# Kernel optimization log

Measured on AMD Instinct MI355X. Metric: run time of the kernel, lower is better.

## Reference

```python
import jax, jax.numpy as jnp
import numpy as np
import math

MU = 5; ETA = 1.0; ITERS = 3
SIGMA_C = 1.0; SIGMA_S = 1.6 * SIGMA_C
SIGMA_M = 3.0; RHO = 0.99; TAU = 0.7
MAX_T = int(math.floor(3 * SIGMA_C))  # 3
MAX_S = int(math.floor(3 * SIGMA_M))  # 9
DELTA = 1.0
B, C, X, Y = 4, 1, 512, 512


def _gpdf(v, sig):
    return math.exp(-v * v / (2.0 * sig * sig)) / (math.sqrt(2.0 * math.pi) * sig)


def _sobel(img):
    k = jnp.array([[-1., -2., -1.], [0., 0., 0.], [1., 2., 1.]], dtype=img.dtype)
    kern = jnp.stack([k, k.T])[:, None]  # [2,1,3,3] OIHW
    return jax.lax.conv_general_dilated(img, kern, (1, 1), [(1, 1), (1, 1)],
                                        dimension_numbers=('NCHW', 'OIHW', 'NCHW'))


def _gather_flat(arr, idx):
    # arr [b,c,x,y], idx int [b,x,y] flattened spatial index (px*Y+py)
    b, c, x, y = arr.shape
    flat = arr.reshape(b, c, x * y)
    idxb = jnp.broadcast_to(idx.reshape(b, 1, x * y), (b, c, x * y))
    return jnp.take_along_axis(flat, idxb, axis=2).reshape(b, c, x, y)


def _safe_norm(v):
    m = jnp.linalg.norm(v, axis=1, keepdims=True)
    return v / jnp.where(m == 0, 1.0, m)


def _etf(images):
    b, c, x, y = images.shape
    sob = _sobel(images)                                   # [b,2,x,y]
    mag = jnp.linalg.norm(sob, axis=1, keepdims=True)      # [b,1,x,y]
    mag = mag / jnp.max(mag)
    mag_p = jnp.pad(mag, ((0, 0), (0, 0), (MU, MU), (MU, MU)))
    sobel_X = mag[:, None]                                 # [b,1,1,x,y]
    tang = _safe_norm(jnp.stack([-sob[:, 1], sob[:, 0]], axis=1))
    K = 2 * MU + 1
    for _ in range(ITERS):
        for ori in ('V', 'H'):
            tang_p = jnp.pad(tang, ((0, 0), (0, 0), (MU, MU), (MU, MU)))
            tang_X = tang[:, None]                         # [b,1,2,x,y]
            if ori == 'V':
                tang_Y = jnp.stack([tang_p[:, :, i:i + x, MU:MU + y] for i in range(K)], axis=1)
                sobel_Y = jnp.stack([mag_p[:, :, i:i + x, MU:MU + y] for i in range(K)], axis=1)
            else:
                tang_Y = jnp.stack([tang_p[:, :, MU:MU + x, i:i + y] for i in range(K)], axis=1)
                sobel_Y = jnp.stack([mag_p[:, :, MU:MU + x, i:i + y] for i in range(K)], axis=1)
            # weight: magnitude term * direction term / 2
            w = (jnp.tanh(ETA * (sobel_Y - sobel_X)) + 1.0) \
                * jnp.sum(tang_X * tang_Y, axis=2, keepdims=True) * 0.5
            tang = _safe_norm(jnp.sum(tang_Y * w, axis=1))
    return tang


def _dog(images, etf):
    b, c, x, y = images.shape
    xi, yi = jnp.meshgrid(jnp.arange(x, dtype=images.dtype),
                          jnp.arange(y, dtype=images.dtype), indexing='ij')
    idx0 = jnp.broadcast_to(jnp.stack([xi, yi])[None], (b, 2, x, y))
    per = jnp.stack([-etf[:, 1], etf[:, 0]], axis=1)       # perpendicular to flow
    dog = jnp.zeros_like(images)
    tw = 0.0
    for t in range(-MAX_T, MAX_T + 1):
        pts = idx0 + DELTA * per * t
        px = jnp.round(jnp.clip(pts[:, 0], 0, x - 1)).astype(jnp.int32)
        py = jnp.round(jnp.clip(pts[:, 1], 0, y - 1)).astype(jnp.int32)
        il = _gather_flat(images, px * y + py)
        gw = _gpdf(t, SIGMA_C) - RHO * _gpdf(t, SIGMA_S)
        tw += gw
        dog = dog + il * gw
    return dog / tw


def _fdog_float(images):
    b, c, x, y = images.shape
    etf = _etf(images)
    dog = _dog(images, etf)
    fdog = jnp.zeros_like(images)
    tw = 0.0
    xi, yi = jnp.meshgrid(jnp.arange(x, dtype=jnp.int32),
                          jnp.arange(y, dtype=jnp.int32), indexing='ij')
    for s_dir in (-1, 1):
        px = jnp.broadcast_to(xi[None], (b, x, y))
        py = jnp.broadcast_to(yi[None], (b, x, y))
        for s in range(0 if s_dir == 1 else 1, MAX_S + 1):
            if s != 0:
                p_etf = _gather_flat(etf, px * y + py)     # flow at current points
                fx = px.astype(images.dtype) + DELTA * p_etf[:, 0] * s_dir
                fy = py.astype(images.dtype) + DELTA * p_etf[:, 1] * s_dir
                px = jnp.round(jnp.clip(fx, 0, x - 1)).astype(jnp.int32)
                py = jnp.round(jnp.clip(fy, 0, y - 1)).astype(jnp.int32)
            f_s = _gather_flat(dog, px * y + py)
            gw = _gpdf(s, SIGMA_M)
            tw += gw
            fdog = fdog + f_s * gw
    return fdog / tw


def setup_inputs() -> dict:
    key = jax.random.key(0)
    images = jax.random.uniform(key, (B, C, X, Y), dtype=jnp.float32)
    return {"images": images}


def reference(images):
    fdog = _fdog_float(images)
    edges = ~((fdog < 0) & (1.0 + jnp.tanh(fdog) < TAU))
    return edges.astype(jnp.int32)
```

## Files before the change

### kernel.cpp

```cpp
#include <hip/hip_runtime.h>
#include <math.h>

#pragma clang fp contract(off)

#define BN 4
#define SX 512
#define SY 512
#define NPIX (BN * SX * SY)
#define MU 5
#define MB (1024 * 1024)
#define SOB_BLOCKS (NPIX / 1024)

struct DogW  { float g[7];  float tw; };
struct FdogW { float g[10]; float tw; };

__device__ __forceinline__ float fast_tanh_f32(float dF) {
    double d = (double)dF;
    double y = fabs(d);
    double t = expm1(2.0 * y);
    double r = t / (t + 2.0);
    if (y > 350.0) r = 1.0;
    return (float)copysign(r, d);
}

__device__ __forceinline__ float img_at(const float* __restrict__ img, int b, int x, int y) {
    if (x < 0 || x >= SX || y < 0 || y >= SY) return 0.0f;
    return img[(size_t)b * SX * SY + (size_t)x * SY + y];
}

__global__ __launch_bounds__(256) void k_sobel(const float* __restrict__ img,
                                               float* __restrict__ mag,
                                               float2* __restrict__ tang,
                                               float* __restrict__ partial) {
#pragma clang fp contract(off)
    int tid = threadIdx.x;
    size_t pixbase = (size_t)blockIdx.x * 1024 + (size_t)tid * 4;
    int b  = (int)(pixbase >> 18);
    int p  = (int)(pixbase & 262143);
    int xi = p >> 9;
    int yi = p & 511;
    size_t base = (size_t)b * SX * SY;
    size_t idx  = base + (size_t)xi * SY + yi;

    bool xm = (xi - 1 >= 0);
    bool xp = (xi + 1 < SX);
    const float* rowm = img + base + (size_t)(xi - 1) * SY;
    const float* row0 = img + base + (size_t)xi * SY;
    const float* rowp = img + base + (size_t)(xi + 1) * SY;

    float4 a4 = make_float4(0.f, 0.f, 0.f, 0.f);
    float4 c4 = make_float4(0.f, 0.f, 0.f, 0.f);
    float4 b4 = *(const float4*)(row0 + yi);
    if (xm) a4 = *(const float4*)(rowm + yi);
    if (xp) c4 = *(const float4*)(rowp + yi);

    float aL = 0.f, aR = 0.f, bL = 0.f, bR = 0.f, cL = 0.f, cR = 0.f;
    if (yi > 0) {
        bL = row0[yi - 1];
        if (xm) aL = rowm[yi - 1];
        if (xp) cL = rowp[yi - 1];
    }
    if (yi + 4 < SY) {
        bR = row0[yi + 4];
        if (xm) aR = rowm[yi + 4];
        if (xp) cR = rowp[yi + 4];
    }

    float a[6] = { aL, a4.x, a4.y, a4.z, a4.w, aR };
    float bb[6] = { bL, b4.x, b4.y, b4.z, b4.w, bR };
    float c[6] = { cL, c4.x, c4.y, c4.z, c4.w, cR };

    float4 m4;
    float4 t01, t23;
    float wm = 0.0f;
#pragma unroll
    for (int j = 0; j < 4; ++j) {
        float v00 = a[j];
        float v01 = a[j + 1];
        float v02 = a[j + 2];
        float v10 = bb[j];
        float v12 = bb[j + 2];
        float v20 = c[j];
        float v21 = c[j + 1];
        float v22 = c[j + 2];

        float s0 = (-1.0f * v00);
        s0 = s0 + (-2.0f * v01);
        s0 = s0 + (-1.0f * v02);
        s0 = s0 + ( 1.0f * v20);
        s0 = s0 + ( 2.0f * v21);
        s0 = s0 + ( 1.0f * v22);
        float s1 = (-1.0f * v00);
        s1 = s1 + ( 1.0f * v02);
        s1 = s1 + (-2.0f * v10);
        s1 = s1 + ( 2.0f * v12);
        s1 = s1 + (-1.0f * v20);
        s1 = s1 + ( 1.0f * v22);

        float m = sqrtf((s0 * s0) + (s1 * s1));
        float tx = -s1, ty = s0;
        float n = sqrtf((tx * tx) + (ty * ty));
        float d = (n == 0.0f) ? 1.0f : n;
        float ex = tx / d;
        float ey = ty / d;

        (&m4.x)[j] = m;
        if (j == 0) { t01.x = ex; t01.y = ey; }
        if (j == 1) { t01.z = ex; t01.w = ey; }
        if (j == 2) { t23.x = ex; t23.y = ey; }
        if (j == 3) { t23.z = ex; t23.w = ey; }
        wm = fmaxf(wm, m);
    }
    *(float4*)(mag + idx) = m4;
    ((float4*)(tang + idx))[0] = t01;
    ((float4*)(tang + idx))[1] = t23;

    for (int off = 32; off > 0; off >>= 1) wm = fmaxf(wm, __shfl_down(wm, off, 64));
    __shared__ float red[4];
    int lane = tid & 63;
    int wid  = tid >> 6;
    if (lane == 0) red[wid] = wm;
    __syncthreads();
    if (tid == 0)
        partial[blockIdx.x] = fmaxf(fmaxf(red[0], red[1]), fmaxf(red[2], red[3]));
}

__global__ void k_reduce(const float* __restrict__ partial, unsigned int* __restrict__ maxbits) {
    float m = 0.0f;
    for (int i = threadIdx.x; i < SOB_BLOCKS; i += 256) m = fmaxf(m, partial[i]);
    for (int off = 32; off > 0; off >>= 1) m = fmaxf(m, __shfl_down(m, off, 64));
    __shared__ float red[4];
    int lane = threadIdx.x & 63;
    int wid  = threadIdx.x >> 6;
    if (lane == 0) red[wid] = m;
    __syncthreads();
    if (threadIdx.x == 0) {
        float bm = fmaxf(fmaxf(red[0], red[1]), fmaxf(red[2], red[3]));
        *maxbits = __float_as_uint(bm);
    }
}

__global__ void k_norm(float* __restrict__ mag, const unsigned int* __restrict__ maxbits) {
    int i = blockIdx.x * blockDim.x + threadIdx.x;
    float mx = __uint_as_float(*maxbits);
    mag[i] = mag[i] / mx;
}

__global__ void k_tanh(const float* __restrict__ mag, const float* __restrict__ partial,
                       float* __restrict__ TV, float* __restrict__ TH) {
#pragma clang fp contract(off)
    int tid = threadIdx.x;
    float m2 = 0.0f;
    for (int i = tid; i < SOB_BLOCKS; i += 256) m2 = fmaxf(m2, partial[i]);
    for (int off = 32; off > 0; off >>= 1) m2 = fmaxf(m2, __shfl_down(m2, off, 64));
    __shared__ float red[4];
    int lane = tid & 63;
    int wid  = tid >> 6;
    if (lane == 0) red[wid] = m2;
    __syncthreads();
    const float mx = fmaxf(fmaxf(red[0], red[1]), fmaxf(red[2], red[3]));

    int yi = blockIdx.x * blockDim.x + tid;
    int xi = blockIdx.y;
    int b  = blockIdx.z;
    size_t base = (size_t)b * SX * SY;
    size_t idx  = base + (size_t)xi * SY + yi;
    float cm = mag[idx] / mx;
#pragma unroll
    for (int k = 1; k <= 5; ++k) {
        if (xi + k < SX) {
            float nm = mag[idx + (size_t)k * SY] / mx;
            TV[(size_t)(k - 1) * NPIX + idx] = fast_tanh_f32(nm - cm);
        }
    }
#pragma unroll
    for (int k = 1; k <= 5; ++k) {
        if (yi + k < SY) {
            float nm = mag[idx + k] / mx;
            TH[(size_t)(k - 1) * NPIX + idx] = fast_tanh_f32(nm - cm);
        }
    }
}

#define VTY 32
#define VTX 16
__global__ __launch_bounds__(256) void k_etf_v(const float2* __restrict__ tsrc,
                                               float2* __restrict__ tdst,
                                               const float* __restrict__ TV) {
#pragma clang fp contract(off)
    int ty  = threadIdx.x & 31;
    int txw = threadIdx.x >> 5;
    int y0 = blockIdx.x * VTY;
    int x0 = blockIdx.y * VTX;
    int b  = blockIdx.z;
    size_t base = (size_t)b * SX * SY;

    __shared__ __align__(16) float2 sT[VTX + 2 * MU][VTY];
    __shared__ __align__(16) float  sTV[5][VTX + MU][VTY];

    int tid = threadIdx.x;
    for (int i = tid; i < (VTX + 2 * MU) * (VTY / 4) * 2; i += 256) {
        int r = i >> 4;
        int c = i & 15;
        int gx = x0 - MU + r;
        if (gx >= 0 && gx < SX)
            ((float4*)&sT[r][0])[c] = ((const float4*)(tsrc + base + (size_t)gx * SY + y0))[c];
    }
    for (int i = tid; i < 5 * (VTX + MU) * (VTY / 4); i += 256) {
        int j   = i / ((VTX + MU) * (VTY / 4));
        int rem = i - j * ((VTX + MU) * (VTY / 4));
        int r   = rem >> 3;
        int c   = rem & 7;
        int gx  = x0 - MU + r;
        if (gx >= 0 && gx < SX)
            ((float4*)&sTV[j][r][0])[c] =
                ((const float4*)(TV + (size_t)j * NPIX + base + (size_t)gx * SY + y0))[c];
    }
    __syncthreads();

    int yi = y0 + ty;
#pragma unroll
    for (int sub = 0; sub < 2; ++sub) {
        int tx = txw + (sub << 3);
        int xi = x0 + tx;
        size_t idx = base + (size_t)xi * SY + yi;

        float2 ct = sT[tx + MU][ty];
        float sx = 0.0f, sy = 0.0f;
#pragma unroll
        for (int k = -MU; k <= MU; ++k) {
            int nx = xi + k;
            if (nx < 0 || nx >= SX) continue;
            float2 nt = sT[tx + MU + k][ty];
            float th;
            if (k > 0)      th =  sTV[k - 1][tx + MU][ty];
            else if (k < 0) th = -sTV[-k - 1][tx + MU + k][ty];
            else            th =  0.0f;
            float dot = (ct.x * nt.x) + (ct.y * nt.y);
            float w   = ((th + 1.0f) * dot) * 0.5f;
            sx = sx + (nt.x * w);
            sy = sy + (nt.y * w);
        }
        float n = sqrtf((sx * sx) + (sy * sy));
        float d = (n == 0.0f) ? 1.0f : n;
        tdst[idx] = make_float2(sx / d, sy / d);
    }
}

__global__ __launch_bounds__(256) void k_etf_h(const float2* __restrict__ tsrc,
                                               float2* __restrict__ tdst,
                                               const float* __restrict__ TH,
                                               const float* __restrict__ img,
                                               float* __restrict__ dogout,
                                               DogW dw, int do_dog) {
#pragma clang fp contract(off)
    int tid = threadIdx.x;
    int xi  = blockIdx.y;
    int b   = blockIdx.z;
    size_t base    = (size_t)b * SX * SY;
    size_t rowbase = base + (size_t)xi * SY;

    __shared__ __align__(16) float2 sT[SY];
    __shared__ __align__(16) float  sTH[5][SY];

    ((float4*)sT)[tid] = ((const float4*)(tsrc + rowbase))[tid];
    for (int i = tid; i < 5 * (SY / 4); i += 256) {
        int j = i >> 7;
        int c = i & 127;
        ((float4*)&sTH[0][0])[i] = ((const float4*)(TH + (size_t)j * NPIX + rowbase))[c];
    }
    __syncthreads();

#pragma unroll
    for (int half = 0; half < 2; ++half) {
        int yi = tid + half * 256;
        float2 ct = sT[yi];
        float sx = 0.0f, sy = 0.0f;
#pragma unroll
        for (int k = -MU; k <= MU; ++k) {
            int ny = yi + k;
            if (ny < 0 || ny >= SY) continue;
            float2 nt = sT[ny];
            float th;
            if (k > 0)      th =  sTH[k - 1][yi];
            else if (k < 0) th = -sTH[-k - 1][ny];
            else            th =  0.0f;
            float dot = (ct.x * nt.x) + (ct.y * nt.y);
            float w   = ((th + 1.0f) * dot) * 0.5f;
            sx = sx + (nt.x * w);
            sy = sy + (nt.y * w);
        }
        float n = sqrtf((sx * sx) + (sy * sy));
        float d = (n == 0.0f) ? 1.0f : n;
        float ex = sx / d;
        float ey = sy / d;
        tdst[rowbase + yi] = make_float2(ex, ey);

        if (do_dog) {
            float perx = -ey;
            float pery =  ex;
            float xf = (float)xi, yf = (float)yi;
            float acc = 0.0f;
#pragma unroll
            for (int t = -3; t <= 3; ++t) {
                float tf  = (float)t;
                float ptx = xf + (perx * tf);
                float pty = yf + (pery * tf);
                int px = (int)rintf(fminf(fmaxf(ptx, 0.0f), (float)(SX - 1)));
                int py = (int)rintf(fminf(fmaxf(pty, 0.0f), (float)(SY - 1)));
                float il = img[base + (size_t)px * SY + py];
                acc = acc + (il * dw.g[t + 3]);
            }
            dogout[rowbase + yi] = acc / dw.tw;
        }
    }
}

__global__ void k_etf(const float2* __restrict__ tsrc, float2* __restrict__ tdst,
                      const float* __restrict__ mag, int vert) {
#pragma clang fp contract(off)
    int yi = blockIdx.x * blockDim.x + threadIdx.x;
    int xi = blockIdx.y;
    int b  = blockIdx.z;
    size_t base = (size_t)b * SX * SY;
    size_t idx  = base + (size_t)xi * SY + yi;

    float  cm = mag[idx];
    float2 ct = tsrc[idx];

    float sx = 0.0f, sy = 0.0f;
    for (int k = -MU; k <= MU; ++k) {
        int nx = xi + (vert ? k : 0);
        int ny = yi + (vert ? 0 : k);
        if (nx < 0 || nx >= SX || ny < 0 || ny >= SY) continue;
        size_t nidx = base + (size_t)nx * SY + ny;
        float  nm = mag[nidx];
        float2 nt = tsrc[nidx];
        float dot = (ct.x * nt.x) + (ct.y * nt.y);
        float th  = (float)tanh((double)(nm - cm));
        float w   = ((th + 1.0f) * dot) * 0.5f;
        sx = sx + (nt.x * w);
        sy = sy + (nt.y * w);
    }
    float n = sqrtf((sx * sx) + (sy * sy));
    float d = (n == 0.0f) ? 1.0f : n;
    tdst[idx] = make_float2(sx / d, sy / d);
}

__global__ void k_dog(const float* __restrict__ img, const float2* __restrict__ etf,
                      float* __restrict__ dog, DogW w) {
#pragma clang fp contract(off)
    int yi = blockIdx.x * blockDim.x + threadIdx.x;
    int xi = blockIdx.y;
    int b  = blockIdx.z;
    size_t base = (size_t)b * SX * SY;
    size_t idx  = base + (size_t)xi * SY + yi;

    float2 e = etf[idx];
    float perx = -e.y;
    float pery =  e.x;
    float xf = (float)xi, yf = (float)yi;

    float acc = 0.0f;
#pragma unroll
    for (int t = -3; t <= 3; ++t) {
        float tf  = (float)t;
        float ptx = xf + (perx * tf);
        float pty = yf + (pery * tf);
        int px = (int)rintf(fminf(fmaxf(ptx, 0.0f), (float)(SX - 1)));
        int py = (int)rintf(fminf(fmaxf(pty, 0.0f), (float)(SY - 1)));
        float il = img[base + (size_t)px * SY + py];
        acc = acc + (il * w.g[t + 3]);
    }
    dog[idx] = acc / w.tw;
}

__global__ void k_fdog(const float* __restrict__ dog, const float2* __restrict__ etf,
                       int* __restrict__ out, FdogW w) {
#pragma clang fp contract(off)
    int yi = blockIdx.x * blockDim.x + threadIdx.x;
    int xi = blockIdx.y;
    int b  = blockIdx.z;
    size_t base = (size_t)b * SX * SY;
    size_t idx  = base + (size_t)xi * SY + yi;

    float d1[9];
    float d2[10];
    float2 e0 = etf[idx];
    float2 e1 = e0, e2 = e0;
    int p1x = xi, p1y = yi;
    int p2x = xi, p2y = yi;
    d2[0] = dog[idx];

#pragma unroll
    for (int s = 1; s <= 9; ++s) {
        float fx1 = (float)p1x + (e1.x * -1.0f);
        float fy1 = (float)p1y + (e1.y * -1.0f);
        p1x = (int)rintf(fminf(fmaxf(fx1, 0.0f), (float)(SX - 1)));
        p1y = (int)rintf(fminf(fmaxf(fy1, 0.0f), (float)(SY - 1)));
        size_t i1 = base + (size_t)p1x * SY + p1y;
        float fx2 = (float)p2x + (e2.x * 1.0f);
        float fy2 = (float)p2y + (e2.y * 1.0f);
        p2x = (int)rintf(fminf(fmaxf(fx2, 0.0f), (float)(SX - 1)));
        p2y = (int)rintf(fminf(fmaxf(fy2, 0.0f), (float)(SY - 1)));
        size_t i2 = base + (size_t)p2x * SY + p2y;

        d1[s - 1] = dog[i1];
        d2[s]     = dog[i2];
        if (s < 9) {
            e1 = etf[i1];
            e2 = etf[i2];
        }
    }

    float acc = 0.0f;
#pragma unroll
    for (int s = 1; s <= 9; ++s) acc = acc + (d1[s - 1] * w.g[s]);
    acc = acc + (d2[0] * w.g[0]);
#pragma unroll
    for (int s = 1; s <= 9; ++s) acc = acc + (d2[s] * w.g[s]);

    float fv = acc / w.tw;
    float th = 1.0f + fast_tanh_f32(fv);
    out[idx] = ((fv < 0.0f) && (th < 0.7f)) ? 0 : 1;
}

static double gpdf(double v, double sig) {
    return exp(-(v * v) / (2.0 * sig * sig)) / (sqrt(2.0 * M_PI) * sig);
}

extern "C" void kernel_launch(void* const* d_in, const int* in_sizes, int n_in,
                              void* d_out, int out_size, void* d_ws, size_t ws_size,
                              hipStream_t stream) {
    const float* img = (const float*)d_in[0];
    int* out = (int*)d_out;
    char* ws = (char*)d_ws;

    const size_t need = (size_t)60 * MB + SOB_BLOCKS * sizeof(float) + 4;
    bool fast = ws_size >= need;

    float*  mag = (float*)(ws);
    float2* tA  = (float2*)(ws + (size_t)4  * MB);
    float2* tB  = (float2*)(ws + (size_t)12 * MB);
    float*  TV  = (float*)(ws + (size_t)20 * MB);
    float*  TH  = (float*)(ws + (size_t)40 * MB);
    size_t  tail = fast ? (size_t)60 * MB : (size_t)20 * MB;
    float*        partial = (float*)(ws + tail);
    unsigned int* maxbits = (unsigned int*)(ws + tail + SOB_BLOCKS * sizeof(float));

    dim3 blk(256, 1, 1);
    dim3 grd(SY / 256, SX, BN);
    dim3 vgrd(SY / VTY, SX / VTX, BN);
    dim3 hgrd(1, SX, BN);

    DogW dw;
    {
        double tw = 0.0;
        for (int t = -3; t <= 3; ++t) {
            double g = gpdf((double)t, 1.0) - 0.99 * gpdf((double)t, 1.6);
            dw.g[t + 3] = (float)g;
            tw += g;
        }
        dw.tw = (float)tw;
    }
    FdogW fw;
    {
        for (int s = 0; s <= 9; ++s) fw.g[s] = (float)gpdf((double)s, 3.0);
        double tw = 0.0;
        for (int s = 1; s <= 9; ++s) tw += gpdf((double)s, 3.0);
        for (int s = 0; s <= 9; ++s) tw += gpdf((double)s, 3.0);
        fw.tw = (float)tw;
    }

    k_sobel<<<dim3(SOB_BLOCKS, 1, 1), blk, 0, stream>>>(img, mag, tA, partial);

    float2* src = tA;
    float2* dst = tB;
    if (fast) {
        float* dogbuf = mag;
        k_tanh<<<grd, blk, 0, stream>>>(mag, partial, TV, TH);
        for (int it = 0; it < 3; ++it) {
            k_etf_v<<<vgrd, blk, 0, stream>>>(src, dst, TV);
            { float2* t = src; src = dst; dst = t; }
            k_etf_h<<<hgrd, blk, 0, stream>>>(src, dst, TH, img, dogbuf, dw, it == 2);
            { float2* t = src; src = dst; dst = t; }
        }
        k_fdog<<<grd, blk, 0, stream>>>(dogbuf, src, out, fw);
    } else {
        k_reduce<<<1, 256, 0, stream>>>(partial, maxbits);
        k_norm<<<NPIX / 256, 256, 0, stream>>>(mag, maxbits);
        for (int it = 0; it < 3; ++it) {
            k_etf<<<grd, blk, 0, stream>>>(src, dst, mag, 1);
            { float2* t = src; src = dst; dst = t; }
            k_etf<<<grd, blk, 0, stream>>>(src, dst, mag, 0);
            { float2* t = src; src = dst; dst = t; }
        }
        float* dogbuf = (src == tA) ? (float*)tB : (float*)tA;
        k_dog<<<grd, blk, 0, stream>>>(img, src, dogbuf, dw);
        k_fdog<<<grd, blk, 0, stream>>>(dogbuf, src, out, fw);
    }
}
```

Baseline: 189.4 us.

## Fuse tanh weight precompute into first ETF passes and widen Sobel per-thread work

```diff
diff --git a/kernel.cpp b/kernel.cpp
--- a/kernel.cpp
+++ b/kernel.cpp
@@ -9,7 +9,7 @@
 #define NPIX (BN * SX * SY)
 #define MU 5
 #define MB (1024 * 1024)
-#define SOB_BLOCKS (NPIX / 1024)
+#define SOB_BLOCKS (NPIX / 2048)
 
 struct DogW  { float g[7];  float tw; };
 struct FdogW { float g[10]; float tw; };
@@ -34,7 +34,7 @@
                                                float* __restrict__ partial) {
 #pragma clang fp contract(off)
     int tid = threadIdx.x;
-    size_t pixbase = (size_t)blockIdx.x * 1024 + (size_t)tid * 4;
+    size_t pixbase = (size_t)blockIdx.x * 2048 + (size_t)tid * 8;
     int b  = (int)(pixbase >> 18);
     int p  = (int)(pixbase & 262143);
     int xi = p >> 9;
@@ -48,11 +48,12 @@
     const float* row0 = img + base + (size_t)xi * SY;
     const float* rowp = img + base + (size_t)(xi + 1) * SY;
 
-    float4 a4 = make_float4(0.f, 0.f, 0.f, 0.f);
-    float4 c4 = make_float4(0.f, 0.f, 0.f, 0.f);
-    float4 b4 = *(const float4*)(row0 + yi);
-    if (xm) a4 = *(const float4*)(rowm + yi);
-    if (xp) c4 = *(const float4*)(rowp + yi);
+    float4 a4a = make_float4(0.f,0.f,0.f,0.f), a4b = make_float4(0.f,0.f,0.f,0.f);
+    float4 c4a = make_float4(0.f,0.f,0.f,0.f), c4b = make_float4(0.f,0.f,0.f,0.f);
+    float4 b4a = *(const float4*)(row0 + yi);
+    float4 b4b = *(const float4*)(row0 + yi + 4);
+    if (xm) { a4a = *(const float4*)(rowm + yi); a4b = *(const float4*)(rowm + yi + 4); }
+    if (xp) { c4a = *(const float4*)(rowp + yi); c4b = *(const float4*)(rowp + yi + 4); }
 
     float aL = 0.f, aR = 0.f, bL = 0.f, bR = 0.f, cL = 0.f, cR = 0.f;
     if (yi > 0) {
@@ -60,21 +61,21 @@
         if (xm) aL = rowm[yi - 1];
         if (xp) cL = rowp[yi - 1];
     }
-    if (yi + 4 < SY) {
-        bR = row0[yi + 4];
-        if (xm) aR = rowm[yi + 4];
-        if (xp) cR = rowp[yi + 4];
-    }
-
-    float a[6] = { aL, a4.x, a4.y, a4.z, a4.w, aR };
-    float bb[6] = { bL, b4.x, b4.y, b4.z, b4.w, bR };
-    float c[6] = { cL, c4.x, c4.y, c4.z, c4.w, cR };
-
-    float4 m4;
-    float4 t01, t23;
+    if (yi + 8 < SY) {
+        bR = row0[yi + 8];
+        if (xm) aR = rowm[yi + 8];
+        if (xp) cR = rowp[yi + 8];
+    }
+
+    float a[10]  = { aL, a4a.x, a4a.y, a4a.z, a4a.w, a4b.x, a4b.y, a4b.z, a4b.w, aR };
+    float bb[10] = { bL, b4a.x, b4a.y, b4a.z, b4a.w, b4b.x, b4b.y, b4b.z, b4b.w, bR };
+    float c[10]  = { cL, c4a.x, c4a.y, c4a.z, c4a.w, c4b.x, c4b.y, c4b.z, c4b.w, cR };
+
+    float m8[8];
+    float tg[16];
     float wm = 0.0f;
 #pragma unroll
-    for (int j = 0; j < 4; ++j) {
+    for (int j = 0; j < 8; ++j) {
         float v00 = a[j];
         float v01 = a[j + 1];
         float v02 = a[j + 2];
@@ -101,19 +102,16 @@
         float tx = -s1, ty = s0;
         float n = sqrtf((tx * tx) + (ty * ty));
         float d = (n == 0.0f) ? 1.0f : n;
-        float ex = tx / d;
-        float ey = ty / d;
-
-        (&m4.x)[j] = m;
-        if (j == 0) { t01.x = ex; t01.y = ey; }
-        if (j == 1) { t01.z = ex; t01.w = ey; }
-        if (j == 2) { t23.x = ex; t23.y = ey; }
-        if (j == 3) { t23.z = ex; t23.w = ey; }
+        m8[j] = m;
+        tg[2 * j]     = tx / d;
+        tg[2 * j + 1] = ty / d;
         wm = fmaxf(wm, m);
     }
-    *(float4*)(mag + idx) = m4;
-    ((float4*)(tang + idx))[0] = t01;
-    ((float4*)(tang + idx))[1] = t23;
+    ((float4*)(mag + idx))[0] = make_float4(m8[0], m8[1], m8[2], m8[3]);
+    ((float4*)(mag + idx))[1] = make_float4(m8[4], m8[5], m8[6], m8[7]);
+#pragma unroll
+    for (int q = 0; q < 4; ++q)
+        ((float4*)(tang + idx))[q] = make_float4(tg[4*q], tg[4*q+1], tg[4*q+2], tg[4*q+3]);
 
     for (int off = 32; off > 0; off >>= 1) wm = fmaxf(wm, __shfl_down(wm, off, 64));
     __shared__ float red[4];
@@ -146,44 +144,159 @@
     mag[i] = mag[i] / mx;
 }
 
-__global__ void k_tanh(const float* __restrict__ mag, const float* __restrict__ partial,
-                       float* __restrict__ TV, float* __restrict__ TH) {
-#pragma clang fp contract(off)
+#define VTY 32
+#define VTX 16
+
+__global__ __launch_bounds__(256) void k_etf_v1(const float2* __restrict__ tsrc,
+                                                float2* __restrict__ tdst,
+                                                const float* __restrict__ mag,
+                                                const float* __restrict__ partial,
+                                                float* __restrict__ TV) {
+#pragma clang fp contract(off)
+    int ty  = threadIdx.x & 31;
+    int txw = threadIdx.x >> 5;
+    int y0 = blockIdx.x * VTY;
+    int x0 = blockIdx.y * VTX;
+    int b  = blockIdx.z;
+    size_t base = (size_t)b * SX * SY;
+
+    __shared__ __align__(16) float2 sT[VTX + 2 * MU][VTY];
+    __shared__ __align__(16) float  sM[VTX + 2 * MU][VTY];
+    __shared__ __align__(16) float  sTV[5][VTX + MU][VTY];
+    __shared__ float red[4];
+
     int tid = threadIdx.x;
+    for (int i = tid; i < (VTX + 2 * MU) * (VTY / 4) * 2; i += 256) {
+        int r = i >> 4;
+        int c = i & 15;
+        int gx = x0 - MU + r;
+        if (gx >= 0 && gx < SX)
+            ((float4*)&sT[r][0])[c] = ((const float4*)(tsrc + base + (size_t)gx * SY + y0))[c];
+    }
+    for (int i = tid; i < (VTX + 2 * MU) * (VTY / 4); i += 256) {
+        int r = i >> 3;
+        int c = i & 7;
+        int gx = x0 - MU + r;
+        if (gx >= 0 && gx < SX)
+            ((float4*)&sM[r][0])[c] = ((const float4*)(mag + base + (size_t)gx * SY + y0))[c];
+    }
     float m2 = 0.0f;
     for (int i = tid; i < SOB_BLOCKS; i += 256) m2 = fmaxf(m2, partial[i]);
     for (int off = 32; off > 0; off >>= 1) m2 = fmaxf(m2, __shfl_down(m2, off, 64));
+    if ((tid & 63) == 0) red[tid >> 6] = m2;
+    __syncthreads();
+    const float mx = fmaxf(fmaxf(red[0], red[1]), fmaxf(red[2], red[3]));
+
+    for (int i = tid; i < 5 * (VTX + MU) * VTY; i += 256) {
+        int j   = i / ((VTX + MU) * VTY);
+        int rem = i - j * ((VTX + MU) * VTY);
+        int r   = rem >> 5;
+        int c   = rem & 31;
+        float nm = sM[r + j + 1][c] / mx;
+        float cm = sM[r][c] / mx;
+        float val = fast_tanh_f32(nm - cm);
+        sTV[j][r][c] = val;
+        int gx = x0 - MU + r;
+        if (gx >= 0 && gx < SX)
+            TV[(size_t)j * NPIX + base + (size_t)gx * SY + (y0 + c)] = val;
+    }
+    __syncthreads();
+
+    int yi = y0 + ty;
+#pragma unroll
+    for (int sub = 0; sub < 2; ++sub) {
+        int tx = txw + (sub << 3);
+        int xi = x0 + tx;
+        size_t idx = base + (size_t)xi * SY + yi;
+
+        float2 ct = sT[tx + MU][ty];
+        float sx = 0.0f, sy = 0.0f;
+#pragma unroll
+        for (int k = -MU; k <= MU; ++k) {
+            int nx = xi + k;
+            if (nx < 0 || nx >= SX) continue;
+            float2 nt = sT[tx + MU + k][ty];
+            float th;
+            if (k > 0)      th =  sTV[k - 1][tx + MU][ty];
+            else if (k < 0) th = -sTV[-k - 1][tx + MU + k][ty];
+            else            th =  0.0f;
+            float dot = (ct.x * nt.x) + (ct.y * nt.y);
+            float w   = ((th + 1.0f) * dot) * 0.5f;
+            sx = sx + (nt.x * w);
+            sy = sy + (nt.y * w);
+        }
+        float n = sqrtf((sx * sx) + (sy * sy));
+        float d = (n == 0.0f) ? 1.0f : n;
+        tdst[idx] = make_float2(sx / d, sy / d);
+    }
+}
+
+__global__ __launch_bounds__(256) void k_etf_h1(const float2* __restrict__ tsrc,
+                                                float2* __restrict__ tdst,
+                                                const float* __restrict__ mag,
+                                                const float* __restrict__ partial,
+                                                float* __restrict__ TH) {
+#pragma clang fp contract(off)
+    int tid = threadIdx.x;
+    int xi  = blockIdx.y;
+    int b   = blockIdx.z;
+    size_t base    = (size_t)b * SX * SY;
+    size_t rowbase = base + (size_t)xi * SY;
+
+    __shared__ __align__(16) float2 sT[SY];
+    __shared__ __align__(16) float  sMr[SY];
+    __shared__ __align__(16) float  sTH[5][SY];
     __shared__ float red[4];
-    int lane = tid & 63;
-    int wid  = tid >> 6;
-    if (lane == 0) red[wid] = m2;
+
+    ((float4*)sT)[tid] = ((const float4*)(tsrc + rowbase))[tid];
+    for (int i = tid; i < SY / 4; i += 256)
+        ((float4*)sMr)[i] = ((const float4*)(mag + rowbase))[i];
+
+    float m2 = 0.0f;
+    for (int i = tid; i < SOB_BLOCKS; i += 256) m2 = fmaxf(m2, partial[i]);
+    for (int off = 32; off > 0; off >>= 1) m2 = fmaxf(m2, __shfl_down(m2, off, 64));
+    if ((tid & 63) == 0) red[tid >> 6] = m2;
     __syncthreads();
     const float mx = fmaxf(fmaxf(red[0], red[1]), fmaxf(red[2], red[3]));
 
-    int yi = blockIdx.x * blockDim.x + tid;
-    int xi = blockIdx.y;
-    int b  = blockIdx.z;
-    size_t base = (size_t)b * SX * SY;
-    size_t idx  = base + (size_t)xi * SY + yi;
-    float cm = mag[idx] / mx;
-#pragma unroll
-    for (int k = 1; k <= 5; ++k) {
-        if (xi + k < SX) {
-            float nm = mag[idx + (size_t)k * SY] / mx;
-            TV[(size_t)(k - 1) * NPIX + idx] = fast_tanh_f32(nm - cm);
-        }
-    }
-#pragma unroll
-    for (int k = 1; k <= 5; ++k) {
-        if (yi + k < SY) {
-            float nm = mag[idx + k] / mx;
-            TH[(size_t)(k - 1) * NPIX + idx] = fast_tanh_f32(nm - cm);
-        }
-    }
-}
-
-#define VTY 32
-#define VTX 16
+    for (int i = tid; i < 5 * SY; i += 256) {
+        int j = i >> 9;
+        int y = i & 511;
+        if (y + j + 1 < SY) {
+            float nm = sMr[y + j + 1] / mx;
+            float cm = sMr[y] / mx;
+            float val = fast_tanh_f32(nm - cm);
+            sTH[j][y] = val;
+            TH[(size_t)j * NPIX + rowbase + y] = val;
+        }
+    }
+    __syncthreads();
+
+#pragma unroll
+    for (int half = 0; half < 2; ++half) {
+        int yi = tid + half * 256;
+        float2 ct = sT[yi];
+        float sx = 0.0f, sy = 0.0f;
+#pragma unroll
+        for (int k = -MU; k <= MU; ++k) {
+            int ny = yi + k;
+            if (ny < 0 || ny >= SY) continue;
+            float2 nt = sT[ny];
+            float th;
+            if (k > 0)      th =  sTH[k - 1][yi];
+            else if (k < 0) th = -sTH[-k - 1][ny];
+            else            th =  0.0f;
+            float dot = (ct.x * nt.x) + (ct.y * nt.y);
+            float w   = ((th + 1.0f) * dot) * 0.5f;
+            sx = sx + (nt.x * w);
+            sy = sy + (nt.y * w);
+        }
+        float n = sqrtf((sx * sx) + (sy * sy));
+        float d = (n == 0.0f) ? 1.0f : n;
+        tdst[rowbase + yi] = make_float2(sx / d, sy / d);
+    }
+}
+
 __global__ __launch_bounds__(256) void k_etf_v(const float2* __restrict__ tsrc,
                                                float2* __restrict__ tdst,
                                                const float* __restrict__ TV) {
@@ -478,8 +591,11 @@
     float2* dst = tB;
     if (fast) {
         float* dogbuf = mag;
-        k_tanh<<<grd, blk, 0, stream>>>(mag, partial, TV, TH);
-        for (int it = 0; it < 3; ++it) {
+        k_etf_v1<<<vgrd, blk, 0, stream>>>(src, dst, mag, partial, TV);
+        { float2* t = src; src = dst; dst = t; }
+        k_etf_h1<<<hgrd, blk, 0, stream>>>(src, dst, mag, partial, TH);
+        { float2* t = src; src = dst; dst = t; }
+        for (int it = 1; it < 3; ++it) {
             k_etf_v<<<vgrd, blk, 0, stream>>>(src, dst, TV);
             { float2* t = src; src = dst; dst = t; }
             k_etf_h<<<hgrd, blk, 0, stream>>>(src, dst, TH, img, dogbuf, dw, it == 2);
```

After: 194.3 us. +2.6%, slower.
